# Kernel optimization log

Measured on AMD Instinct MI355X. Metric: run time of the kernel, lower is better.

## Reference

```python
import jax, jax.numpy as jnp
import numpy as np

B, S, H, L, A, V, NL = 16, 256, 768, 12, 12, 30522, 9
DH = H // A
FF = 4 * H


def _ln(x, g, b):
    m = x.mean(-1, keepdims=True)
    v = jnp.var(x, axis=-1, keepdims=True)
    return (x - m) * jax.lax.rsqrt(v + 1e-12) * g + b


def setup_inputs() -> dict:
    key = jax.random.key(0)
    ks = jax.random.split(key, 16)
    n = lambda k, shape: jax.random.normal(k, shape, jnp.float32) * 0.02
    return {
        "input_word_ids": jax.random.randint(ks[0], (B, S), 0, V, jnp.int32),
        "input_mask": jnp.ones((B, S), jnp.int32),
        "input_type_ids": jnp.zeros((B, S), jnp.int32),
        "valid_mask": jax.random.randint(ks[1], (B, S), 0, 2, jnp.int32),
        "word_emb": n(ks[2], (V, H)),
        "pos_emb": n(ks[3], (S, H)),
        "type_emb": n(ks[4], (2, H)),
        "emb_ln_g": jnp.ones((H,), jnp.float32),
        "emb_ln_b": jnp.zeros((H,), jnp.float32),
        "Wq": n(ks[5], (L, H, H)), "bq": jnp.zeros((L, H), jnp.float32),
        "Wk": n(ks[6], (L, H, H)), "bk": jnp.zeros((L, H), jnp.float32),
        "Wv": n(ks[7], (L, H, H)), "bv": jnp.zeros((L, H), jnp.float32),
        "Wo": n(ks[8], (L, H, H)), "bo": jnp.zeros((L, H), jnp.float32),
        "attn_ln_g": jnp.ones((L, H), jnp.float32),
        "attn_ln_b": jnp.zeros((L, H), jnp.float32),
        "W1": n(ks[9], (L, H, FF)), "b1": jnp.zeros((L, FF), jnp.float32),
        "W2": n(ks[10], (L, FF, H)), "b2": jnp.zeros((L, H), jnp.float32),
        "ffn_ln_g": jnp.ones((L, H), jnp.float32),
        "ffn_ln_b": jnp.zeros((L, H), jnp.float32),
        "cls_W": n(ks[11], (H, NL)),
        "cls_b": jnp.zeros((NL,), jnp.float32),
    }


def reference(input_word_ids, input_mask, input_type_ids, valid_mask,
              word_emb, pos_emb, type_emb, emb_ln_g, emb_ln_b,
              Wq, bq, Wk, bk, Wv, bv, Wo, bo, attn_ln_g, attn_ln_b,
              W1, b1, W2, b2, ffn_ln_g, ffn_ln_b, cls_W, cls_b):
    # --- BERT embeddings ---
    x = word_emb[input_word_ids] + pos_emb[None, :, :] + type_emb[input_type_ids]
    x = _ln(x, emb_ln_g, emb_ln_b)
    amask = (1.0 - input_mask.astype(jnp.float32))[:, None, None, :] * -10000.0

    # --- 12 post-LN transformer layers via scan over stacked weights ---
    def block(x, p):
        wq, bq_, wk, bk_, wv, bv_, wo, bo_, ag, ab, w1, b1_, w2, b2_, fg, fb = p
        q = (x @ wq + bq_).reshape(B, S, A, DH)
        k = (x @ wk + bk_).reshape(B, S, A, DH)
        v = (x @ wv + bv_).reshape(B, S, A, DH)
        s = jnp.einsum('bqhd,bkhd->bhqk', q, k) * (1.0 / float(np.sqrt(DH))) + amask
        a = jax.nn.softmax(s, axis=-1)
        ctx = jnp.einsum('bhqk,bkhd->bqhd', a, v).reshape(B, S, H)
        x = _ln(x + ctx @ wo + bo_, ag, ab)
        h = jax.nn.gelu(x @ w1 + b1_)
        x = _ln(x + h @ w2 + b2_, fg, fb)
        return x, None

    x, _ = jax.lax.scan(block, x, (Wq, bq, Wk, bk, Wv, bv, Wo, bo,
                                   attn_ln_g, attn_ln_b, W1, b1, W2, b2,
                                   ffn_ln_g, ffn_ln_b))

    # --- valid-mask token compaction: valid tokens to front, zero pad ---
    # stable argsort moves valid_mask==1 positions to the front, in order
    order = jnp.argsort(1 - valid_mask, axis=1)  # stable by default
    gathered = jnp.take_along_axis(x, order[:, :, None], axis=1)
    counts = valid_mask.sum(axis=1)  # [B]
    keep = (jnp.arange(S)[None, :] < counts[:, None])[:, :, None]
    valid_out = jnp.where(keep, gathered, jnp.zeros((), x.dtype))

    # dropout is identity (training=False default); softmax classifier head
    return jax.nn.softmax(valid_out @ cls_W + cls_b, axis=-1)
```

## Files before the change

kernel.cpp:

```cpp
#include <hip/hip_runtime.h>

#define TOKENS 4096
#define BATCH  16
#define SEQ    256
#define Hdim   768
#define FFdim  3072
#define NHEAD  12
#define NLBL   9
#define NLAYER 12
#define QKVS   2304

typedef unsigned short u16;
typedef __attribute__((ext_vector_type(8))) short short8;
typedef __attribute__((ext_vector_type(4))) float floatx4;

__device__ __forceinline__ float bf2f(u16 u) {
    union { unsigned int i; float f; } c; c.i = ((unsigned int)u) << 16; return c.f;
}
__device__ __forceinline__ u16 f2bf(float f) {
    union { float f; unsigned int i; } c; c.f = f;
    unsigned int u = c.i;
    u = u + 0x7fffu + ((u >> 16) & 1u);
    return (u16)(u >> 16);
}

#define GLOAD16(gp, lp) __builtin_amdgcn_global_load_lds( \
    (__attribute__((address_space(1))) void*)(gp), \
    (__attribute__((address_space(3))) void*)(lp), 16, 0, 0)

__global__ __launch_bounds__(256) void k_conv_all(
    const float* __restrict__ Wq, const float* __restrict__ Wk,
    const float* __restrict__ Wv, const float* __restrict__ Wo,
    const float* __restrict__ W1, const float* __restrict__ W2,
    u16* __restrict__ qkvT, u16* __restrict__ oT,
    u16* __restrict__ w1T, u16* __restrict__ w2T)
{
    const size_t HH = (size_t)768 * 768, HF = (size_t)768 * 3072;
    int bid = blockIdx.x;
    int l = bid / 1728;
    int r = bid - l * 1728;
    const float* src; u16* dst; int K, N, t;
    if (r < 576) {
        int m = r / 144; t = r - m * 144;
        src = ((m == 0) ? Wq : (m == 1) ? Wk : (m == 2) ? Wv : Wo) + l * HH;
        dst = (m < 3) ? (qkvT + (size_t)l * QKVS * 768 + (size_t)m * 768 * 768)
                      : (oT + l * HH);
        K = 768; N = 768;
    } else if (r < 1152) {
        t = r - 576; src = W1 + l * HF; dst = w1T + l * HF; K = 768; N = 3072;
    } else {
        t = r - 1152; src = W2 + l * HF; dst = w2T + l * HF; K = 3072; N = 768;
    }
    int ntn = N >> 6;
    int tk = t / ntn, tn = t - tk * ntn;

    __shared__ float ld[64][65];
    int tid = threadIdx.x;
    int rr = tid >> 4;
    int cc = (tid & 15) * 4;
#pragma unroll
    for (int i = 0; i < 4; i++) {
        int k = tk * 64 + rr + i * 16;
        float4 v = *(const float4*)(src + (size_t)k * N + tn * 64 + cc);
        ld[rr + i * 16][cc + 0] = v.x;
        ld[rr + i * 16][cc + 1] = v.y;
        ld[rr + i * 16][cc + 2] = v.z;
        ld[rr + i * 16][cc + 3] = v.w;
    }
    __syncthreads();
    int n  = tid >> 2;
    int kc = (tid & 3) * 16;
    union { u16 h[16]; uint4 v[2]; } ob;
#pragma unroll
    for (int j = 0; j < 16; j++) ob.h[j] = f2bf(ld[kc + j][n]);
    u16* op = dst + (size_t)(tn * 64 + n) * K + tk * 64 + kc;
    *(uint4*)(op)     = ob.v[0];
    *(uint4*)(op + 8) = ob.v[1];
}

__global__ void k_biascat(const float* __restrict__ bq, const float* __restrict__ bk,
                          const float* __restrict__ bv, float* __restrict__ o)
{
    int l = blockIdx.x, t = threadIdx.x;
    o[l * QKVS + t]        = bq[l * Hdim + t];
    o[l * QKVS + 768 + t]  = bk[l * Hdim + t];
    o[l * QKVS + 1536 + t] = bv[l * Hdim + t];
}

template<int MODE, int BN>
__global__ __launch_bounds__(256) void k_gemm(const u16* __restrict__ Ag, const u16* __restrict__ Bg,
                                              const float* __restrict__ bias, void* __restrict__ outp,
                                              int N, int K)
{
    constexpr int NFR = BN / 32;
    __shared__ u16 As[3][128 * 32];
    __shared__ u16 Bs[3][BN * 32];
    const int tid  = threadIdx.x;
    const int lane = tid & 63, w = tid >> 6;
    const int wr = w >> 1, wc = w & 1;
    const int quad = lane >> 4, l16 = lane & 15;
    const int m0 = blockIdx.y * 128, n0 = blockIdx.x * BN;

    const int r0 = tid >> 2, c0 = (tid & 3) * 8;
    const u16* a0 = Ag + (size_t)(m0 + r0) * K + c0;
    const u16* a1 = a0 + (size_t)64 * K;
    const u16* b0 = Bg + (size_t)(n0 + r0) * K + c0;
    const u16* b1 = b0 + (size_t)64 * K;
    const int lofs0 = w * 512;
    const int lofs1 = 2048 + w * 512;

#define STAGE(kk, sl) do { \
        GLOAD16(a0 + (kk), &As[sl][lofs0]); \
        GLOAD16(a1 + (kk), &As[sl][lofs1]); \
        GLOAD16(b0 + (kk), &Bs[sl][lofs0]); \
        if constexpr (BN == 128) GLOAD16(b1 + (kk), &Bs[sl][lofs1]); \
    } while (0)

    const floatx4 vzero = {0.f, 0.f, 0.f, 0.f};
    floatx4 acc[4][NFR];
#pragma unroll
    for (int i = 0; i < 4; i++)
#pragma unroll
        for (int j = 0; j < NFR; j++) acc[i][j] = vzero;

    const int NT = K >> 5;

    STAGE(0, 0);
    STAGE(32, 1);

    int cur = 0;
    for (int t = 0; t < NT; ++t) {
        int sl = cur + 2; if (sl >= 3) sl -= 3;
        if (t + 2 < NT) {
            STAGE((t + 2) << 5, sl);
            if constexpr (BN == 128) asm volatile("s_waitcnt vmcnt(8)" ::: "memory");
            else                     asm volatile("s_waitcnt vmcnt(6)" ::: "memory");
        } else if (t + 1 < NT) {
            if constexpr (BN == 128) asm volatile("s_waitcnt vmcnt(4)" ::: "memory");
            else                     asm volatile("s_waitcnt vmcnt(3)" ::: "memory");
        } else {
            asm volatile("s_waitcnt vmcnt(0)" ::: "memory");
        }
        __builtin_amdgcn_sched_barrier(0);
        __builtin_amdgcn_s_barrier();
        __builtin_amdgcn_sched_barrier(0);

        const u16* Ab = As[cur];
        const u16* Bb = Bs[cur];
        short8 af[4], bfr[NFR];
#pragma unroll
        for (int mt = 0; mt < 4; mt++)
            af[mt]  = *(const short8*)(Ab + (wr * 64 + mt * 16 + l16) * 32 + quad * 8);
#pragma unroll
        for (int nt = 0; nt < NFR; nt++)
            bfr[nt] = *(const short8*)(Bb + (wc * (BN / 2) + nt * 16 + l16) * 32 + quad * 8);
#pragma unroll
        for (int mt = 0; mt < 4; mt++)
#pragma unroll
            for (int nt = 0; nt < NFR; nt++)
                acc[mt][nt] = __builtin_amdgcn_mfma_f32_16x16x32_bf16(af[mt], bfr[nt], acc[mt][nt], 0, 0, 0);

        __builtin_amdgcn_sched_barrier(0);
        __builtin_amdgcn_s_barrier();
        __builtin_amdgcn_sched_barrier(0);

        cur = (cur == 2) ? 0 : cur + 1;
    }
#undef STAGE

#pragma unroll
    for (int mt = 0; mt < 4; mt++) {
#pragma unroll
        for (int nt = 0; nt < NFR; nt++) {
            int col = n0 + wc * (BN / 2) + nt * 16 + l16;
            float bv = bias[col];
#pragma unroll
            for (int r = 0; r < 4; r++) {
                int row = m0 + wr * 64 + mt * 16 + quad * 4 + r;
                float vv = acc[mt][nt][r] + bv;
                if (MODE == 1) {
                    float t = 0.7978845608028654f * (vv + 0.044715f * vv * vv * vv);
                    vv = 0.5f * vv * (1.0f + tanhf(t));
                }
                if (MODE == 2) ((float*)outp)[(size_t)row * N + col] = vv;
                else          ((u16*)outp)[(size_t)row * N + col] = f2bf(vv);
            }
        }
    }
}

__global__ __launch_bounds__(256) void k_embed(const int* __restrict__ wid, const int* __restrict__ tidv,
                                               const float* __restrict__ we, const float* __restrict__ pe, const float* __restrict__ te,
                                               const float* __restrict__ g, const float* __restrict__ bb,
                                               float* __restrict__ xf, u16* __restrict__ xh)
{
    int i = blockIdx.x; int s = i & 255;
    int t = threadIdx.x;
    int wv = wid[i], tv = tidv[i];
    float e[3]; float sum = 0.f, sq = 0.f;
#pragma unroll
    for (int r = 0; r < 3; r++) {
        int j = t + r * 256;
        float x = we[(size_t)wv * Hdim + j] + pe[s * Hdim + j] + te[tv * Hdim + j];
        e[r] = x; sum += x; sq += x * x;
    }
    __shared__ float red[8];
    for (int off = 32; off; off >>= 1) { sum += __shfl_xor(sum, off); sq += __shfl_xor(sq, off); }
    if ((t & 63) == 0) { red[t >> 6] = sum; red[4 + (t >> 6)] = sq; }
    __syncthreads();
    sum = red[0] + red[1] + red[2] + red[3];
    sq  = red[4] + red[5] + red[6] + red[7];
    float mean = sum * (1.0f / Hdim);
    float var  = sq * (1.0f / Hdim) - mean * mean;
    float rstd = rsqrtf(var + 1e-12f);
#pragma unroll
    for (int r = 0; r < 3; r++) {
        int j = t + r * 256;
        float v = (e[r] - mean) * rstd * g[j] + bb[j];
        xf[(size_t)i * Hdim + j] = v;
        xh[(size_t)i * Hdim + j] = f2bf(v);
    }
}

__global__ __launch_bounds__(256) void k_addln(float* __restrict__ xf, const float* __restrict__ y,
                                               const float* __restrict__ g, const float* __restrict__ bb,
                                               u16* __restrict__ xh)
{
    int i = blockIdx.x; int t = threadIdx.x;
    float e[3]; float sum = 0.f, sq = 0.f;
#pragma unroll
    for (int r = 0; r < 3; r++) {
        int j = t + r * 256;
        float x = xf[(size_t)i * Hdim + j] + y[(size_t)i * Hdim + j];
        e[r] = x; sum += x; sq += x * x;
    }
    __shared__ float red[8];
    for (int off = 32; off; off >>= 1) { sum += __shfl_xor(sum, off); sq += __shfl_xor(sq, off); }
    if ((t & 63) == 0) { red[t >> 6] = sum; red[4 + (t >> 6)] = sq; }
    __syncthreads();
    sum = red[0] + red[1] + red[2] + red[3];
    sq  = red[4] + red[5] + red[6] + red[7];
    float mean = sum * (1.0f / Hdim);
    float var  = sq * (1.0f / Hdim) - mean * mean;
    float rstd = rsqrtf(var + 1e-12f);
#pragma unroll
    for (int r = 0; r < 3; r++) {
        int j = t + r * 256;
        float v = (e[r] - mean) * rstd * g[j] + bb[j];
        xf[(size_t)i * Hdim + j] = v;
        xh[(size_t)i * Hdim + j] = f2bf(v);
    }
}

__global__ __launch_bounds__(256, 2) void k_attn(const u16* __restrict__ qkv, const int* __restrict__ maskg,
                                                 u16* __restrict__ ctx)
{
    __shared__ u16 Vt[64 * 264];
    __shared__ u16 Ps[4 * 64 * 40];
    __shared__ float madd[256];
    int bh = blockIdx.x; int b = bh / NHEAD; int h = bh - b * NHEAD;
    int tid = threadIdx.x; int lane = tid & 63; int w = tid >> 6;
    int quad = lane >> 4, l16 = lane & 15;
    size_t baseq = (size_t)b * SEQ * QKVS + h * 64;
    size_t basec = (size_t)b * SEQ * Hdim + h * 64;

#pragma unroll
    for (int i = 0; i < 8; i++) {
        int c = tid + i * 256; int key = c >> 3; int cc = (c & 7) << 3;
        uint4 vv = *(const uint4*)(qkv + baseq + 1536 + (size_t)key * QKVS + cc);
        const u16* p16 = (const u16*)&vv;
#pragma unroll
        for (int e = 0; e < 8; e++) Vt[(cc + e) * 264 + key] = p16[e];
    }
    madd[tid] = (1.0f - (float)maskg[b * SEQ + tid]) * -10000.0f;
    __syncthreads();

    short8 aq[4][2];
#pragma unroll
    for (int mt = 0; mt < 4; mt++)
#pragma unroll
        for (int kf = 0; kf < 2; kf++)
            aq[mt][kf] = *(const short8*)(qkv + baseq + (size_t)(w * 64 + mt * 16 + l16) * QKVS + kf * 32 + quad * 8);

    const floatx4 vzero = {0.f, 0.f, 0.f, 0.f};
    floatx4 acc[4][4];
    float l_run[4][4];
#pragma unroll
    for (int a = 0; a < 4; a++)
#pragma unroll
        for (int r = 0; r < 4; r++) { acc[a][r] = vzero; l_run[a][r] = 0.f; }

    u16* Pw = &Ps[w * 64 * 40];

    for (int kc = 0; kc < 8; kc++) {
        floatx4 sc[4][2];
#pragma unroll
        for (int mt = 0; mt < 4; mt++) { sc[mt][0] = vzero; sc[mt][1] = vzero; }
#pragma unroll
        for (int kf = 0; kf < 2; kf++) {
            short8 bk_[2];
#pragma unroll
            for (int nt = 0; nt < 2; nt++)
                bk_[nt] = *(const short8*)(qkv + baseq + 768 + (size_t)(kc * 32 + nt * 16 + l16) * QKVS + kf * 32 + quad * 8);
#pragma unroll
            for (int mt = 0; mt < 4; mt++)
#pragma unroll
                for (int nt = 0; nt < 2; nt++)
                    sc[mt][nt] = __builtin_amdgcn_mfma_f32_16x16x32_bf16(aq[mt][kf], bk_[nt], sc[mt][nt], 0, 0, 0);
        }
        float madd0 = madd[kc * 32 + l16];
        float madd1 = madd[kc * 32 + 16 + l16];
#pragma unroll
        for (int mt = 0; mt < 4; mt++) {
#pragma unroll
            for (int r = 0; r < 4; r++) {
                float p0 = __expf(sc[mt][0][r] * 0.125f + madd0);
                float p1 = __expf(sc[mt][1][r] * 0.125f + madd1);
                float ls = p0 + p1;
#pragma unroll
                for (int off = 1; off < 16; off <<= 1) ls += __shfl_xor(ls, off);
                l_run[mt][r] += ls;
                int row = mt * 16 + quad * 4 + r;
                Pw[row * 40 + l16]      = f2bf(p0);
                Pw[row * 40 + 16 + l16] = f2bf(p1);
            }
        }
        short8 ap[4], bv_[4];
#pragma unroll
        for (int nt = 0; nt < 4; nt++)
            bv_[nt] = *(const short8*)(&Vt[(nt * 16 + l16) * 264 + kc * 32 + quad * 8]);
#pragma unroll
        for (int mt = 0; mt < 4; mt++)
            ap[mt] = *(const short8*)(&Pw[(mt * 16 + l16) * 40 + quad * 8]);
#pragma unroll
        for (int mt = 0; mt < 4; mt++)
#pragma unroll
            for (int nt = 0; nt < 4; nt++)
                acc[mt][nt] = __builtin_amdgcn_mfma_f32_16x16x32_bf16(ap[mt], bv_[nt], acc[mt][nt], 0, 0, 0);
    }
#pragma unroll
    for (int mt = 0; mt < 4; mt++)
#pragma unroll
        for (int r = 0; r < 4; r++) {
            float inv = 1.0f / l_run[mt][r];
            int sq_ = w * 64 + mt * 16 + quad * 4 + r;
#pragma unroll
            for (int nt = 0; nt < 4; nt++)
                ctx[basec + (size_t)sq_ * Hdim + nt * 16 + l16] = f2bf(acc[mt][nt][r] * inv);
        }
}

__global__ void k_compact(const int* __restrict__ vm, int* __restrict__ counts, int* __restrict__ srcidx)
{
    int b = blockIdx.x;
    if (threadIdx.x == 0) {
        int c = 0;
        for (int s = 0; s < SEQ; s++)
            if (vm[b * SEQ + s]) { srcidx[b * SEQ + c] = s; c++; }
        counts[b] = c;
    }
}

__global__ __launch_bounds__(256) void k_cls(const u16* __restrict__ x, const int* __restrict__ counts,
                                             const int* __restrict__ srcidx, const float* __restrict__ Wc,
                                             const float* __restrict__ bc, float* __restrict__ out)
{
    int w = threadIdx.x >> 6, lane = threadIdx.x & 63;
    int row = blockIdx.x * 4 + w;
    int b = row >> 8, s = row & 255;
    float acc[NLBL];
#pragma unroll
    for (int n = 0; n < NLBL; n++) acc[n] = 0.f;
    int cnt = counts[b];
    if (s < cnt) {
        int src = srcidx[b * SEQ + s];
        const u16* xr = x + (size_t)(b * SEQ + src) * Hdim;
        for (int j = lane; j < Hdim; j += 64) {
            float xv = bf2f(xr[j]);
#pragma unroll
            for (int n = 0; n < NLBL; n++) acc[n] += xv * Wc[j * NLBL + n];
        }
    }
#pragma unroll
    for (int n = 0; n < NLBL; n++)
        for (int off = 32; off; off >>= 1) acc[n] += __shfl_xor(acc[n], off);
    if (lane == 0) {
        float lg[NLBL]; float mx = -1e30f;
#pragma unroll
        for (int n = 0; n < NLBL; n++) { lg[n] = acc[n] + bc[n]; mx = fmaxf(mx, lg[n]); }
        float se = 0.f;
#pragma unroll
        for (int n = 0; n < NLBL; n++) { lg[n] = __expf(lg[n] - mx); se += lg[n]; }
        float inv = 1.0f / se;
#pragma unroll
        for (int n = 0; n < NLBL; n++) out[(size_t)row * NLBL + n] = lg[n] * inv;
    }
}

extern "C" void kernel_launch(void* const* d_in, const int* in_sizes, int n_in,
                              void* d_out, int out_size, void* d_ws, size_t ws_size,
                              hipStream_t stream)
{
    (void)in_sizes; (void)n_in; (void)out_size; (void)ws_size;
    const int* word_ids = (const int*)d_in[0];
    const int* in_mask  = (const int*)d_in[1];
    const int* type_ids = (const int*)d_in[2];
    const int* valid    = (const int*)d_in[3];
    const float* word_emb = (const float*)d_in[4];
    const float* pos_emb  = (const float*)d_in[5];
    const float* type_emb = (const float*)d_in[6];
    const float* eg = (const float*)d_in[7];
    const float* eb = (const float*)d_in[8];
    const float* Wq = (const float*)d_in[9];  const float* bq = (const float*)d_in[10];
    const float* Wk = (const float*)d_in[11]; const float* bk = (const float*)d_in[12];
    const float* Wv = (const float*)d_in[13]; const float* bv = (const float*)d_in[14];
    const float* Wo = (const float*)d_in[15]; const float* bo = (const float*)d_in[16];
    const float* ag = (const float*)d_in[17]; const float* ab = (const float*)d_in[18];
    const float* W1 = (const float*)d_in[19]; const float* b1 = (const float*)d_in[20];
    const float* W2 = (const float*)d_in[21]; const float* b2 = (const float*)d_in[22];
    const float* fg = (const float*)d_in[23]; const float* fb = (const float*)d_in[24];
    const float* Wc = (const float*)d_in[25]; const float* bc = (const float*)d_in[26];
    float* out = (float*)d_out;

    char* p = (char*)d_ws;
    int* counts = (int*)p;
    int* srcidx = (int*)(p + 1024);
    p += 65536;
    float* x_f32 = (float*)p; p += (size_t)TOKENS * Hdim * 4;
    u16* x_h  = (u16*)p; p += (size_t)TOKENS * Hdim * 2;
    float* tmpf = (float*)p; p += (size_t)TOKENS * Hdim * 4;
    u16* qkv_h = (u16*)p; p += (size_t)TOKENS * QKVS * 2;
    u16* c_h  = (u16*)p; p += (size_t)TOKENS * Hdim * 2;
    u16* h_h  = qkv_h;
    u16* wqkvT = (u16*)p; p += (size_t)NLAYER * QKVS * Hdim * 2;
    u16* woT   = (u16*)p; p += (size_t)NLAYER * Hdim * Hdim * 2;
    u16* w1T   = (u16*)p; p += (size_t)NLAYER * FFdim * Hdim * 2;
    u16* w2T   = (u16*)p; p += (size_t)NLAYER * Hdim * FFdim * 2;
    float* bqkv = (float*)p; p += (size_t)NLAYER * QKVS * 4;

    k_embed<<<TOKENS, 256, 0, stream>>>(word_ids, type_ids, word_emb, pos_emb, type_emb, eg, eb, x_f32, x_h);
    k_compact<<<BATCH, 64, 0, stream>>>(valid, counts, srcidx);
    k_biascat<<<NLAYER, 768, 0, stream>>>(bq, bk, bv, bqkv);
    k_conv_all<<<NLAYER * 1728, 256, 0, stream>>>(Wq, Wk, Wv, Wo, W1, W2, wqkvT, woT, w1T, w2T);

    for (int l = 0; l < NLAYER; l++) {
        size_t HH = (size_t)Hdim * Hdim;
        size_t HF = (size_t)Hdim * FFdim;
        k_gemm<0, 128><<<dim3(18, 32), 256, 0, stream>>>(x_h, wqkvT + (size_t)l * QKVS * Hdim,
                                                         bqkv + l * QKVS, qkv_h, QKVS, Hdim);
        k_attn<<<BATCH * NHEAD, 256, 0, stream>>>(qkv_h, in_mask, c_h);
        k_gemm<2, 64><<<dim3(12, 32), 256, 0, stream>>>(c_h, woT + l * HH, bo + l * Hdim, tmpf, Hdim, Hdim);
        k_addln<<<TOKENS, 256, 0, stream>>>(x_f32, tmpf, ag + l * Hdim, ab + l * Hdim, x_h);
        k_gemm<1, 128><<<dim3(24, 32), 256, 0, stream>>>(x_h, w1T + l * HF, b1 + l * FFdim, h_h, FFdim, Hdim);
        k_gemm<2, 64><<<dim3(12, 32), 256, 0, stream>>>(h_h, w2T + l * HF, b2 + l * Hdim, tmpf, Hdim, FFdim);
        k_addln<<<TOKENS, 256, 0, stream>>>(x_f32, tmpf, fg + l * Hdim, fb + l * Hdim, x_h);
    }
    k_cls<<<TOKENS / 4, 256, 0, stream>>>(x_h, counts, srcidx, Wc, bc, out);
}
```

Measured before the change: 2.644 ms.

## Retile GEMMs to 64x128, split attention query rows, rewrite weight conversion

Every GEMM now uses a single 64x128 block tile with launch bounds asking for four blocks per CU. This roughly doubles the grid (for example 18x64 for the QKV GEMM) so more of the 256 CUs on MI355X have work. Attention is split into two blocks per batch-head, each covering 128 query rows, and occupancy is raised to three blocks. The weight fp32-to-bf16 transpose kernel now has each thread read strided columns directly and write 16-byte bf16 runs, with no shared-memory tile. The cost of the smaller tiles is less operand reuse per block, and each attention block has to reload K and V.

```diff
diff --git a/kernel.cpp b/kernel.cpp
--- a/kernel.cpp
+++ b/kernel.cpp
@@ -37,45 +37,41 @@
 {
     const size_t HH = (size_t)768 * 768, HF = (size_t)768 * 3072;
     int bid = blockIdx.x;
-    int l = bid / 1728;
-    int r = bid - l * 1728;
-    const float* src; u16* dst; int K, N, t;
-    if (r < 576) {
-        int m = r / 144; t = r - m * 144;
-        src = ((m == 0) ? Wq : (m == 1) ? Wk : (m == 2) ? Wv : Wo) + l * HH;
-        dst = (m < 3) ? (qkvT + (size_t)l * QKVS * 768 + (size_t)m * 768 * 768)
-                      : (oT + l * HH);
-        K = 768; N = 768;
-    } else if (r < 1152) {
-        t = r - 576; src = W1 + l * HF; dst = w1T + l * HF; K = 768; N = 3072;
+    int l = bid / 144;
+    int r = bid - l * 144;
+    const float* src; u16* dst; int N, dstride, kb, n0;
+    if (r < 36) {
+        int m = r / 12, s = r - m * 12;
+        src = ((m == 0) ? Wq : (m == 1) ? Wk : Wv) + l * HH;
+        dst = qkvT + (size_t)l * QKVS * Hdim + ((size_t)m * 768 + s * 64) * 768;
+        N = 768; dstride = 768; kb = 0; n0 = s * 64;
+    } else if (r < 48) {
+        int s = r - 36;
+        src = Wo + l * HH; dst = oT + l * HH + (size_t)s * 64 * 768;
+        N = 768; dstride = 768; kb = 0; n0 = s * 64;
+    } else if (r < 96) {
+        int s = r - 48;
+        src = W1 + l * HF; dst = w1T + l * HF + (size_t)s * 64 * 768;
+        N = 3072; dstride = 768; kb = 0; n0 = s * 64;
     } else {
-        t = r - 1152; src = W2 + l * HF; dst = w2T + l * HF; K = 3072; N = 768;
-    }
-    int ntn = N >> 6;
-    int tk = t / ntn, tn = t - tk * ntn;
-
-    __shared__ float ld[64][65];
-    int tid = threadIdx.x;
-    int rr = tid >> 4;
-    int cc = (tid & 15) * 4;
-#pragma unroll
-    for (int i = 0; i < 4; i++) {
-        int k = tk * 64 + rr + i * 16;
-        float4 v = *(const float4*)(src + (size_t)k * N + tn * 64 + cc);
-        ld[rr + i * 16][cc + 0] = v.x;
-        ld[rr + i * 16][cc + 1] = v.y;
-        ld[rr + i * 16][cc + 2] = v.z;
-        ld[rr + i * 16][cc + 3] = v.w;
-    }
-    __syncthreads();
-    int n  = tid >> 2;
-    int kc = (tid & 3) * 16;
-    union { u16 h[16]; uint4 v[2]; } ob;
-#pragma unroll
-    for (int j = 0; j < 16; j++) ob.h[j] = f2bf(ld[kc + j][n]);
-    u16* op = dst + (size_t)(tn * 64 + n) * K + tk * 64 + kc;
-    *(uint4*)(op)     = ob.v[0];
-    *(uint4*)(op + 8) = ob.v[1];
+        int rr = r - 96; int s = rr >> 2; int kc = rr & 3;
+        src = W2 + l * HF; dst = w2T + l * HF + (size_t)s * 64 * 3072;
+        N = 768; dstride = 3072; kb = kc * 768; n0 = s * 64;
+    }
+    int t = threadIdx.x;
+    int kseg = (t & 3) * 8;
+    int n = t >> 2;
+    const float* sp = src + n0 + n;
+    u16* dp = dst + (size_t)n * dstride;
+#pragma unroll 2
+    for (int p = 0; p < 24; ++p) {
+        int k0 = kb + p * 32 + kseg;
+        union { u16 h[8]; uint4 v; } ob;
+#pragma unroll
+        for (int j = 0; j < 8; ++j)
+            ob.h[j] = f2bf(sp[(size_t)(k0 + j) * N]);
+        *(uint4*)(dp + k0) = ob.v;
+    }
 }
 
 __global__ void k_biascat(const float* __restrict__ bq, const float* __restrict__ bk,
@@ -87,41 +83,37 @@
     o[l * QKVS + 1536 + t] = bv[l * Hdim + t];
 }
 
-template<int MODE, int BN>
-__global__ __launch_bounds__(256) void k_gemm(const u16* __restrict__ Ag, const u16* __restrict__ Bg,
-                                              const float* __restrict__ bias, void* __restrict__ outp,
-                                              int N, int K)
-{
-    constexpr int NFR = BN / 32;
-    __shared__ u16 As[3][128 * 32];
-    __shared__ u16 Bs[3][BN * 32];
+template<int MODE>
+__global__ __launch_bounds__(256, 4) void k_gemm(const u16* __restrict__ Ag, const u16* __restrict__ Bg,
+                                                 const float* __restrict__ bias, void* __restrict__ outp,
+                                                 int N, int K)
+{
+    __shared__ u16 As[3][64 * 32];
+    __shared__ u16 Bs[3][128 * 32];
     const int tid  = threadIdx.x;
     const int lane = tid & 63, w = tid >> 6;
     const int wr = w >> 1, wc = w & 1;
     const int quad = lane >> 4, l16 = lane & 15;
-    const int m0 = blockIdx.y * 128, n0 = blockIdx.x * BN;
+    const int m0 = blockIdx.y * 64, n0 = blockIdx.x * 128;
 
     const int r0 = tid >> 2, c0 = (tid & 3) * 8;
     const u16* a0 = Ag + (size_t)(m0 + r0) * K + c0;
-    const u16* a1 = a0 + (size_t)64 * K;
     const u16* b0 = Bg + (size_t)(n0 + r0) * K + c0;
     const u16* b1 = b0 + (size_t)64 * K;
-    const int lofs0 = w * 512;
-    const int lofs1 = 2048 + w * 512;
+    const int lofs = w * 512;
 
 #define STAGE(kk, sl) do { \
-        GLOAD16(a0 + (kk), &As[sl][lofs0]); \
-        GLOAD16(a1 + (kk), &As[sl][lofs1]); \
-        GLOAD16(b0 + (kk), &Bs[sl][lofs0]); \
-        if constexpr (BN == 128) GLOAD16(b1 + (kk), &Bs[sl][lofs1]); \
+        GLOAD16(a0 + (kk), &As[sl][lofs]); \
+        GLOAD16(b0 + (kk), &Bs[sl][lofs]); \
+        GLOAD16(b1 + (kk), &Bs[sl][2048 + lofs]); \
     } while (0)
 
     const floatx4 vzero = {0.f, 0.f, 0.f, 0.f};
-    floatx4 acc[4][NFR];
-#pragma unroll
-    for (int i = 0; i < 4; i++)
-#pragma unroll
-        for (int j = 0; j < NFR; j++) acc[i][j] = vzero;
+    floatx4 acc[2][4];
+#pragma unroll
+    for (int i = 0; i < 2; i++)
+#pragma unroll
+        for (int j = 0; j < 4; j++) acc[i][j] = vzero;
 
     const int NT = K >> 5;
 
@@ -133,11 +125,9 @@
         int sl = cur + 2; if (sl >= 3) sl -= 3;
         if (t + 2 < NT) {
             STAGE((t + 2) << 5, sl);
-            if constexpr (BN == 128) asm volatile("s_waitcnt vmcnt(8)" ::: "memory");
-            else                     asm volatile("s_waitcnt vmcnt(6)" ::: "memory");
+            asm volatile("s_waitcnt vmcnt(6)" ::: "memory");
         } else if (t + 1 < NT) {
-            if constexpr (BN == 128) asm volatile("s_waitcnt vmcnt(4)" ::: "memory");
-            else                     asm volatile("s_waitcnt vmcnt(3)" ::: "memory");
+            asm volatile("s_waitcnt vmcnt(3)" ::: "memory");
         } else {
             asm volatile("s_waitcnt vmcnt(0)" ::: "memory");
         }
@@ -147,17 +137,17 @@
 
         const u16* Ab = As[cur];
         const u16* Bb = Bs[cur];
-        short8 af[4], bfr[NFR];
-#pragma unroll
-        for (int mt = 0; mt < 4; mt++)
-            af[mt]  = *(const short8*)(Ab + (wr * 64 + mt * 16 + l16) * 32 + quad * 8);
-#pragma unroll
-        for (int nt = 0; nt < NFR; nt++)
-            bfr[nt] = *(const short8*)(Bb + (wc * (BN / 2) + nt * 16 + l16) * 32 + quad * 8);
-#pragma unroll
-        for (int mt = 0; mt < 4; mt++)
-#pragma unroll
-            for (int nt = 0; nt < NFR; nt++)
+        short8 af[2], bfr[4];
+#pragma unroll
+        for (int mt = 0; mt < 2; mt++)
+            af[mt]  = *(const short8*)(Ab + (wr * 32 + mt * 16 + l16) * 32 + quad * 8);
+#pragma unroll
+        for (int nt = 0; nt < 4; nt++)
+            bfr[nt] = *(const short8*)(Bb + (wc * 64 + nt * 16 + l16) * 32 + quad * 8);
+#pragma unroll
+        for (int mt = 0; mt < 2; mt++)
+#pragma unroll
+            for (int nt = 0; nt < 4; nt++)
                 acc[mt][nt] = __builtin_amdgcn_mfma_f32_16x16x32_bf16(af[mt], bfr[nt], acc[mt][nt], 0, 0, 0);
 
         __builtin_amdgcn_sched_barrier(0);
@@ -169,14 +159,14 @@
 #undef STAGE
 
 #pragma unroll
-    for (int mt = 0; mt < 4; mt++) {
-#pragma unroll
-        for (int nt = 0; nt < NFR; nt++) {
-            int col = n0 + wc * (BN / 2) + nt * 16 + l16;
+    for (int mt = 0; mt < 2; mt++) {
+#pragma unroll
+        for (int nt = 0; nt < 4; nt++) {
+            int col = n0 + wc * 64 + nt * 16 + l16;
             float bv = bias[col];
 #pragma unroll
             for (int r = 0; r < 4; r++) {
-                int row = m0 + wr * 64 + mt * 16 + quad * 4 + r;
+                int row = m0 + wr * 32 + mt * 16 + quad * 4 + r;
                 float vv = acc[mt][nt][r] + bv;
                 if (MODE == 1) {
                     float t = 0.7978845608028654f * (vv + 0.044715f * vv * vv * vv);
@@ -252,13 +242,15 @@
     }
 }
 
-__global__ __launch_bounds__(256, 2) void k_attn(const u16* __restrict__ qkv, const int* __restrict__ maskg,
+__global__ __launch_bounds__(256, 3) void k_attn(const u16* __restrict__ qkv, const int* __restrict__ maskg,
                                                  u16* __restrict__ ctx)
 {
     __shared__ u16 Vt[64 * 264];
-    __shared__ u16 Ps[4 * 64 * 40];
+    __shared__ u16 Ps[4 * 32 * 40];
     __shared__ float madd[256];
-    int bh = blockIdx.x; int b = bh / NHEAD; int h = bh - b * NHEAD;
+    int bid = blockIdx.x;
+    int half = bid & 1; int bh = bid >> 1;
+    int b = bh / NHEAD; int h = bh - b * NHEAD;
     int tid = threadIdx.x; int lane = tid & 63; int w = tid >> 6;
     int quad = lane >> 4, l16 = lane & 15;
     size_t baseq = (size_t)b * SEQ * QKVS + h * 64;
@@ -275,27 +267,27 @@
     madd[tid] = (1.0f - (float)maskg[b * SEQ + tid]) * -10000.0f;
     __syncthreads();
 
-    short8 aq[4][2];
-#pragma unroll
-    for (int mt = 0; mt < 4; mt++)
+    short8 aq[2][2];
+#pragma unroll
+    for (int mt = 0; mt < 2; mt++)
 #pragma unroll
         for (int kf = 0; kf < 2; kf++)
-            aq[mt][kf] = *(const short8*)(qkv + baseq + (size_t)(w * 64 + mt * 16 + l16) * QKVS + kf * 32 + quad * 8);
+            aq[mt][kf] = *(const short8*)(qkv + baseq + (size_t)(half * 128 + w * 32 + mt * 16 + l16) * QKVS + kf * 32 + quad * 8);
 
     const floatx4 vzero = {0.f, 0.f, 0.f, 0.f};
-    floatx4 acc[4][4];
-    float l_run[4][4];
-#pragma unroll
-    for (int a = 0; a < 4; a++)
+    floatx4 acc[2][4];
+    float l_run[2][4];
+#pragma unroll
+    for (int a = 0; a < 2; a++)
 #pragma unroll
         for (int r = 0; r < 4; r++) { acc[a][r] = vzero; l_run[a][r] = 0.f; }
 
-    u16* Pw = &Ps[w * 64 * 40];
+    u16* Pw = &Ps[w * 32 * 40];
 
     for (int kc = 0; kc < 8; kc++) {
-        floatx4 sc[4][2];
-#pragma unroll
-        for (int mt = 0; mt < 4; mt++) { sc[mt][0] = vzero; sc[mt][1] = vzero; }
+        floatx4 sc[2][2];
+#pragma unroll
+        for (int mt = 0; mt < 2; mt++) { sc[mt][0] = vzero; sc[mt][1] = vzero; }
 #pragma unroll
         for (int kf = 0; kf < 2; kf++) {
             short8 bk_[2];
@@ -303,7 +295,7 @@
             for (int nt = 0; nt < 2; nt++)
                 bk_[nt] = *(const short8*)(qkv + baseq + 768 + (size_t)(kc * 32 + nt * 16 + l16) * QKVS + kf * 32 + quad * 8);
 #pragma unroll
-            for (int mt = 0; mt < 4; mt++)
+            for (int mt = 0; mt < 2; mt++)
 #pragma unroll
                 for (int nt = 0; nt < 2; nt++)
                     sc[mt][nt] = __builtin_amdgcn_mfma_f32_16x16x32_bf16(aq[mt][kf], bk_[nt], sc[mt][nt], 0, 0, 0);
@@ -311,7 +303,7 @@
         float madd0 = madd[kc * 32 + l16];
         float madd1 = madd[kc * 32 + 16 + l16];
 #pragma unroll
-        for (int mt = 0; mt < 4; mt++) {
+        for (int mt = 0; mt < 2; mt++) {
 #pragma unroll
             for (int r = 0; r < 4; r++) {
                 float p0 = __expf(sc[mt][0][r] * 0.125f + madd0);
@@ -325,25 +317,25 @@
                 Pw[row * 40 + 16 + l16] = f2bf(p1);
             }
         }
-        short8 ap[4], bv_[4];
+        short8 ap[2], bv_[4];
 #pragma unroll
         for (int nt = 0; nt < 4; nt++)
             bv_[nt] = *(const short8*)(&Vt[(nt * 16 + l16) * 264 + kc * 32 + quad * 8]);
 #pragma unroll
-        for (int mt = 0; mt < 4; mt++)
+        for (int mt = 0; mt < 2; mt++)
             ap[mt] = *(const short8*)(&Pw[(mt * 16 + l16) * 40 + quad * 8]);
 #pragma unroll
-        for (int mt = 0; mt < 4; mt++)
+        for (int mt = 0; mt < 2; mt++)
 #pragma unroll
             for (int nt = 0; nt < 4; nt++)
                 acc[mt][nt] = __builtin_amdgcn_mfma_f32_16x16x32_bf16(ap[mt], bv_[nt], acc[mt][nt], 0, 0, 0);
     }
 #pragma unroll
-    for (int mt = 0; mt < 4; mt++)
+    for (int mt = 0; mt < 2; mt++)
 #pragma unroll
         for (int r = 0; r < 4; r++) {
             float inv = 1.0f / l_run[mt][r];
-            int sq_ = w * 64 + mt * 16 + quad * 4 + r;
+            int sq_ = half * 128 + w * 32 + mt * 16 + quad * 4 + r;
 #pragma unroll
             for (int nt = 0; nt < 4; nt++)
                 ctx[basec + (size_t)sq_ * Hdim + nt * 16 + l16] = f2bf(acc[mt][nt][r] * inv);
@@ -441,18 +433,18 @@
     k_embed<<<TOKENS, 256, 0, stream>>>(word_ids, type_ids, word_emb, pos_emb, type_emb, eg, eb, x_f32, x_h);
     k_compact<<<BATCH, 64, 0, stream>>>(valid, counts, srcidx);
     k_biascat<<<NLAYER, 768, 0, stream>>>(bq, bk, bv, bqkv);
-    k_conv_all<<<NLAYER * 1728, 256, 0, stream>>>(Wq, Wk, Wv, Wo, W1, W2, wqkvT, woT, w1T, w2T);
+    k_conv_all<<<NLAYER * 144, 256, 0, stream>>>(Wq, Wk, Wv, Wo, W1, W2, wqkvT, woT, w1T, w2T);
 
     for (int l = 0; l < NLAYER; l++) {
         size_t HH = (size_t)Hdim * Hdim;
         size_t HF = (size_t)Hdim * FFdim;
-        k_gemm<0, 128><<<dim3(18, 32), 256, 0, stream>>>(x_h, wqkvT + (size_t)l * QKVS * Hdim,
-                                                         bqkv + l * QKVS, qkv_h, QKVS, Hdim);
-        k_attn<<<BATCH * NHEAD, 256, 0, stream>>>(qkv_h, in_mask, c_h);
-        k_gemm<2, 64><<<dim3(12, 32), 256, 0, stream>>>(c_h, woT + l * HH, bo + l * Hdim, tmpf, Hdim, Hdim);
+        k_gemm<0><<<dim3(18, 64), 256, 0, stream>>>(x_h, wqkvT + (size_t)l * QKVS * Hdim,
+                                                    bqkv + l * QKVS, qkv_h, QKVS, Hdim);
+        k_attn<<<BATCH * NHEAD * 2, 256, 0, stream>>>(qkv_h, in_mask, c_h);
+        k_gemm<2><<<dim3(6, 64), 256, 0, stream>>>(c_h, woT + l * HH, bo + l * Hdim, tmpf, Hdim, Hdim);
         k_addln<<<TOKENS, 256, 0, stream>>>(x_f32, tmpf, ag + l * Hdim, ab + l * Hdim, x_h);
-        k_gemm<1, 128><<<dim3(24, 32), 256, 0, stream>>>(x_h, w1T + l * HF, b1 + l * FFdim, h_h, FFdim, Hdim);
-        k_gemm<2, 64><<<dim3(12, 32), 256, 0, stream>>>(h_h, w2T + l * HF, b2 + l * Hdim, tmpf, Hdim, FFdim);
+        k_gemm<1><<<dim3(24, 64), 256, 0, stream>>>(x_h, w1T + l * HF, b1 + l * FFdim, h_h, FFdim, Hdim);
+        k_gemm<2><<<dim3(6, 64), 256, 0, stream>>>(h_h, w2T + l * HF, b2 + l * Hdim, tmpf, Hdim, FFdim);
         k_addln<<<TOKENS, 256, 0, stream>>>(x_f32, tmpf, fg + l * Hdim, fb + l * Hdim, x_h);
     }
     k_cls<<<TOKENS / 4, 256, 0, stream>>>(x_h, counts, srcidx, Wc, bc, out);
```

Result: slower. 3.092 ms (+16.9%).
